# Optimization experiments

Hardware: AMD Instinct MI355X
Metric: run time of the kernel (lower is better)

Reference implementation:

```python
import jax, jax.numpy as jnp
import numpy as np

B, T, D, H = 2, 2048, 1024, 16
NEG = -65504.0


def setup_inputs() -> dict:
    key = jax.random.key(0)
    ks = jax.random.split(key, 12)
    std = float(np.sqrt(2.0 / (D + D)))  # xavier_normal for square weights
    inp = {
        'q': jax.random.normal(ks[0], (B, T, D), jnp.float32),
        'k': jax.random.normal(ks[1], (B, T, D), jnp.float32),
        'v': jax.random.normal(ks[2], (B, T, D), jnp.float32),
        'mask': jax.random.randint(ks[3], (B, T), 0, 2, jnp.int32),
        # weights stored as (in, out) so y = x @ W + b
        'Wq': jax.random.normal(ks[4], (D, D), jnp.float32) * std,
        'bq': jnp.zeros((D,), jnp.float32),
        'Wk': jax.random.normal(ks[5], (D, D), jnp.float32) * std,
        'bk': jnp.zeros((D,), jnp.float32),
        'Wv': jax.random.normal(ks[6], (D, D), jnp.float32) * std,
        'bv': jnp.zeros((D,), jnp.float32),
        'Wo': jax.random.normal(ks[7], (D, D), jnp.float32) * std,
        'bo': jnp.zeros((D,), jnp.float32),
    }
    return inp


def reference(q, k, v, mask, Wq, bq, Wk, bk, Wv, bv, Wo, bo):
    b, t, _ = q.shape
    dim_a = Wq.shape[1]
    dh = dim_a // H
    # projections, then split into heads: (b, t, H, dh)
    qh = (q @ Wq + bq).reshape(b, t, H, dh)
    kh = (k @ Wk + bk).reshape(b, t, H, dh)
    vh = (v @ Wv + bv).reshape(b, t, H, dh)
    # NOTE: module scales by 1/sqrt(dim_a) with the FULL dim_a, not per-head
    a = jnp.einsum('bthd,bshd->bhts', qh, kh) / jnp.sqrt(jnp.float32(dim_a))
    # 2D mask broadcasts over query positions: (b, 1, 1, t_keys)
    a = jnp.where(mask[:, None, None, :] == 0, NEG, a)
    a = jax.nn.softmax(a, axis=-1)  # dropout_prob=0 (eval mode)
    o = jnp.einsum('bhts,bshd->bthd', a, vh).reshape(b, t, dim_a)
    return o @ Wo + bo
```

## Files before the change

kernel.cpp:

```cpp
#include <hip/hip_runtime.h>
#include <hip/hip_bf16.h>
#include <math.h>

#define B_ 2
#define T_ 2048
#define D_ 1024
#define H_ 16
#define QSCALE (0.03125f * 1.44269504088896f)

typedef _Float16 f16;
using f16x4 = __attribute__((ext_vector_type(4))) _Float16;
using f16x8 = __attribute__((ext_vector_type(8))) _Float16;
using f32x4 = __attribute__((ext_vector_type(4))) float;

__device__ __forceinline__ void gl16(const void* g, void* l) {
  __builtin_amdgcn_global_load_lds(
      (__attribute__((address_space(1))) void*)g,
      (__attribute__((address_space(3))) void*)l, 16, 0, 0);
}

__global__ __launch_bounds__(256) void prep(
    const float* __restrict__ q, const float* __restrict__ k,
    const float* __restrict__ v, const int* __restrict__ mask,
    const float* __restrict__ Wq, const float* __restrict__ Wk,
    const float* __restrict__ Wv, const float* __restrict__ Wo,
    const float* __restrict__ bq, const float* __restrict__ bk,
    const float* __restrict__ bv, const float* __restrict__ bo,
    f16* __restrict__ xqkv, f16* __restrict__ Wt, float* __restrict__ bias,
    int* __restrict__ idx, int* __restrict__ inv, int* __restrict__ nk,
    f16* __restrict__ khc) {
  __shared__ float sh[64][65];
  const int bid = blockIdx.x;
  const int tid = threadIdx.x;

  if (bid < 6144) {
    const int z = bid / 2048;
    const float* src = (z == 0) ? q : (z == 1) ? k : v;
    const size_t i = ((size_t)(bid % 2048) * 256 + tid) * 8;
    float4 a = *(const float4*)(src + i);
    float4 b = *(const float4*)(src + i + 4);
    f16x8 o;
    o[0] = (f16)a.x; o[1] = (f16)a.y; o[2] = (f16)a.z; o[3] = (f16)a.w;
    o[4] = (f16)b.x; o[5] = (f16)b.y; o[6] = (f16)b.z; o[7] = (f16)b.w;
    *(f16x8*)(xqkv + (size_t)z * 4194304 + i) = o;
  } else if (bid < 7168) {
    const int id = bid - 6144;
    const int z = id >> 8;
    const int k0 = ((id >> 4) & 15) * 64, n0 = (id & 15) * 64;
    const float* W = (z == 0) ? Wq : (z == 1) ? Wk : (z == 2) ? Wv : Wo;
    const int r = tid >> 2, c0 = (tid & 3) * 16;
#pragma unroll
    for (int i = 0; i < 4; ++i)
      *(float4*)&sh[r][c0 + 4 * i] =
          *(const float4*)&W[(size_t)(k0 + r) * 1024 + n0 + c0 + 4 * i];
    __syncthreads();
    f16 tmp[16];
#pragma unroll
    for (int i = 0; i < 16; ++i) tmp[i] = (f16)sh[c0 + i][r];
    f16* dst = Wt + (size_t)z * 1048576 + (size_t)(n0 + r) * 1024 + k0 + c0;
    *(f16x8*)dst = *(f16x8*)&tmp[0];
    *(f16x8*)(dst + 8) = *(f16x8*)&tmp[8];
  } else if (bid < 7184) {
    const int i = (bid - 7168) * 256 + tid;
    const int z = i >> 10;
    const float* s = (z == 0) ? bq : (z == 1) ? bk : (z == 2) ? bv : bo;
    bias[i] = s[i & 1023];
  } else {
    const int b = bid - 7184;
    int* cnt = (int*)sh;
    int loc[8];
    int c = 0;
#pragma unroll
    for (int i = 0; i < 8; ++i) {
      loc[i] = mask[b * T_ + tid * 8 + i];
      c += loc[i];
    }
    cnt[tid] = c;
    __syncthreads();
    for (int off = 1; off < 256; off <<= 1) {
      int vsh = (tid >= off) ? cnt[tid - off] : 0;
      __syncthreads();
      cnt[tid] += vsh;
      __syncthreads();
    }
    int pos = cnt[tid] - c;
#pragma unroll
    for (int i = 0; i < 8; ++i) {
      const int t = tid * 8 + i;
      if (loc[i]) {
        idx[b * T_ + pos] = t;
        inv[b * T_ + t] = pos;
        ++pos;
      } else {
        inv[b * T_ + t] = -1;
      }
    }
    const int n = cnt[255];
    if (tid == 255) nk[b] = n;
    const int nkt = (n + 63) >> 6;
    const int npadrows = (nkt << 6) - n;
    uint4 z4 = {0u, 0u, 0u, 0u};
    f16* base = khc + ((size_t)b * T_ + n) * D_;
    for (int i = tid; i < npadrows * 128; i += 256)
      *(uint4*)(base + (size_t)i * 8) = z4;
  }
}

template <int TM, typename OT>
__global__ __launch_bounds__(256) void gemm_bt(
    const f16* __restrict__ Xb, const f16* __restrict__ Wtb,
    const float* __restrict__ biasb, void* __restrict__ C0,
    void* __restrict__ C1, void* __restrict__ C2,
    const int* __restrict__ inv, int M, int N, int K, float qscale) {
  constexpr int FM = TM / 32;
  __shared__ __align__(16) f16 As[TM * 32];
  __shared__ __align__(16) f16 Bs[128 * 32];
  const int z = blockIdx.z;
  const f16* X  = Xb  + (size_t)z * M * K;
  const f16* Wt = Wtb + (size_t)z * N * K;
  const float* bias = biasb + (size_t)z * N;
  OT* C = (OT*)((z == 0) ? C0 : (z == 1) ? C1 : C2);
  const float scl = (z == 0) ? qscale : 1.f;

  const int tid = threadIdx.x;
  const int wave = tid >> 6, lane = tid & 63;
  const int quad = lane >> 4, l16 = lane & 15;
  const int wm = wave & 1, wn = wave >> 1;
  const int m0 = blockIdx.y * TM, n0 = blockIdx.x * 128;

  f32x4 acc[FM][4] = {};

  const f16* asrc = X  + (size_t)(m0 + (tid >> 2)) * K + (tid & 3) * 8;
  const f16* bsrc = Wt + (size_t)(n0 + (tid >> 2)) * K + (tid & 3) * 8;
  char* aldst = (char*)As + tid * 16;
  char* bldst = (char*)Bs + tid * 16;
  const size_t rstep = (size_t)64 * K;

  const int NK = K >> 5;
  for (int kt = 0; kt < NK; ++kt) {
    if (kt) __syncthreads();
    gl16(asrc, aldst);
    if constexpr (TM == 128) gl16(asrc + rstep, aldst + 4096);
    gl16(bsrc, bldst);
    gl16(bsrc + rstep, bldst + 4096);
    asrc += 32; bsrc += 32;
    __syncthreads();

    f16x8 af[FM], bf[4];
#pragma unroll
    for (int t = 0; t < FM; ++t)
      af[t] = *(const f16x8*)&As[((TM / 2) * wm + 16 * t + l16) * 32 + quad * 8];
#pragma unroll
    for (int t = 0; t < 4; ++t)
      bf[t] = *(const f16x8*)&Bs[(64 * wn + 16 * t + l16) * 32 + quad * 8];
#pragma unroll
    for (int i = 0; i < FM; ++i)
#pragma unroll
      for (int j = 0; j < 4; ++j)
        acc[i][j] = __builtin_amdgcn_mfma_f32_16x16x32_f16(af[i], bf[j], acc[i][j], 0, 0, 0);
  }

  const int cm = m0 + (TM / 2) * wm + 4 * quad;
  const int cn = n0 + 64 * wn + l16;
  float bv[4];
#pragma unroll
  for (int tn = 0; tn < 4; ++tn) bv[tn] = bias[cn + 16 * tn];

  if (inv != nullptr && z == 1) {
    const int bb = m0 >> 11;
#pragma unroll
    for (int tm = 0; tm < FM; ++tm) {
#pragma unroll
      for (int r = 0; r < 4; ++r) {
        const int m = cm + 16 * tm + r;
        const int j = inv[m];
        if (j >= 0) {
          OT* row = C + ((size_t)(bb << 11) + j) * N;
#pragma unroll
          for (int tn = 0; tn < 4; ++tn)
            row[cn + 16 * tn] = (OT)(acc[tm][tn][r] + bv[tn]);
        }
      }
    }
  } else {
#pragma unroll
    for (int tm = 0; tm < FM; ++tm)
#pragma unroll
      for (int r = 0; r < 4; ++r) {
        OT* row = C + (size_t)(cm + 16 * tm + r) * N;
#pragma unroll
        for (int tn = 0; tn < 4; ++tn)
          row[cn + 16 * tn] = (OT)((acc[tm][tn][r] + bv[tn]) * scl);
      }
  }
}

__global__ __launch_bounds__(256) void vtrans(
    const f16* __restrict__ vh, const int* __restrict__ idx,
    const int* __restrict__ nk, f16* __restrict__ vhT) {
  const int tt = blockIdx.x, bh = blockIdx.y;
  const int b = bh >> 4, h = bh & 15;
  const int n = nk[b];
  const int nkt = (n + 63) >> 6;
  if (tt >= nkt) return;
  __shared__ f16 t[64][72];
  const int tid = threadIdx.x;
  const int r = tid >> 2, cq = 16 * (tid & 3);

  const int j = tt * 64 + r;
  uint4 v0 = {0u, 0u, 0u, 0u}, v1 = {0u, 0u, 0u, 0u};
  if (j < n) {
    const int tsrc = idx[b * T_ + j];
    const uint4* src = (const uint4*)(vh + ((size_t)b * T_ + tsrc) * D_ + h * 64 + cq);
    v0 = src[0]; v1 = src[1];
  }
  *(uint4*)&t[r][cq]     = v0;
  *(uint4*)&t[r][cq + 8] = v1;
  __syncthreads();

  f16 tmp[16];
#pragma unroll
  for (int xx = 0; xx < 16; ++xx) {
    int x = (xx + r) & 15;
    tmp[x] = t[cq + x][r];
  }
  f16* dst = vhT + ((size_t)bh * 64 + r) * T_ + tt * 64 + cq;
  *(uint4*)&dst[0] = *(uint4*)&tmp[0];
  *(uint4*)&dst[8] = *(uint4*)&tmp[8];
}

__global__ __launch_bounds__(256) void attn_mfma(
    const f16* __restrict__ qh, const f16* __restrict__ khc,
    const f16* __restrict__ vhT, const int* __restrict__ nkd,
    f16* __restrict__ oat) {
  __shared__ f16 Ks[64][72];
  __shared__ f16 Vt[64][72];
  __shared__ f16 Ps[4][32][72];

  const int qt = blockIdx.x, bh = blockIdx.y;
  const int b = bh >> 4, h = bh & 15;
  const int tid = threadIdx.x;
  const int wave = tid >> 6, lane = tid & 63;
  const int quad = lane >> 4, l16 = lane & 15;
  const int sr = tid >> 2, sq = 16 * (tid & 3);

  const int n = nkd[b];
  const int nkt = (n + 63) >> 6;
  const int npad = (nkt << 6) - n;

  f16x8 qf[2][2];
#pragma unroll
  for (int gq = 0; gq < 2; ++gq) {
    const f16* qp = qh + ((size_t)(b * T_ + qt * 128 + wave * 32 + 16 * gq + l16)) * D_ + h * 64 + quad * 8;
    qf[gq][0] = *(const f16x8*)qp;
    qf[gq][1] = *(const f16x8*)(qp + 32);
  }

  float lsum[2] = {0.f, 0.f};
  f32x4 o[2][4] = {};

  const f16* kbase = khc + (size_t)b * T_ * D_ + h * 64;
  const f16* vbase = vhT + ((size_t)bh * 64 + sr) * T_;

  uint4 kr0, kr1, vr0, vr1;
  auto load_kv = [&](int kt) {
    const uint4* ks = (const uint4*)(kbase + (size_t)(kt * 64 + sr) * D_ + sq);
    kr0 = ks[0]; kr1 = ks[1];
    const uint4* vs = (const uint4*)(vbase + kt * 64 + sq);
    vr0 = vs[0]; vr1 = vs[1];
  };
  if (nkt > 0) load_kv(0);

  for (int kt = 0; kt < nkt; ++kt) {
    *(uint4*)&Ks[sr][sq]     = kr0;
    *(uint4*)&Ks[sr][sq + 8] = kr1;
    *(uint4*)&Vt[sr][sq]     = vr0;
    *(uint4*)&Vt[sr][sq + 8] = vr1;
    __syncthreads();
    if (kt + 1 < nkt) load_kv(kt + 1);

#pragma unroll
    for (int tn = 0; tn < 4; ++tn) {
      f16x8 kf0 = *(const f16x8*)&Ks[16 * tn + l16][quad * 8];
      f16x8 kf1 = *(const f16x8*)&Ks[16 * tn + l16][32 + quad * 8];
#pragma unroll
      for (int gq = 0; gq < 2; ++gq) {
        f32x4 s = {0.f, 0.f, 0.f, 0.f};
        s = __builtin_amdgcn_mfma_f32_16x16x32_f16(kf0, qf[gq][0], s, 0, 0, 0);
        s = __builtin_amdgcn_mfma_f32_16x16x32_f16(kf1, qf[gq][1], s, 0, 0, 0);
        float p0 = exp2f(s[0]), p1 = exp2f(s[1]);
        float p2 = exp2f(s[2]), p3 = exp2f(s[3]);
        lsum[gq] += (p0 + p1) + (p2 + p3);
        f16x4 pk;
        pk[0] = (f16)p0; pk[1] = (f16)p1; pk[2] = (f16)p2; pk[3] = (f16)p3;
        *(f16x4*)&Ps[wave][16 * gq + l16][16 * tn + 4 * quad] = pk;
      }
    }

    f16x8 pf[2][2];
#pragma unroll
    for (int gq = 0; gq < 2; ++gq) {
      pf[gq][0] = *(const f16x8*)&Ps[wave][16 * gq + l16][quad * 8];
      pf[gq][1] = *(const f16x8*)&Ps[wave][16 * gq + l16][32 + quad * 8];
    }
#pragma unroll
    for (int t = 0; t < 4; ++t) {
      f16x8 vf0 = *(const f16x8*)&Vt[16 * t + l16][quad * 8];
      f16x8 vf1 = *(const f16x8*)&Vt[16 * t + l16][32 + quad * 8];
#pragma unroll
      for (int gq = 0; gq < 2; ++gq) {
        o[gq][t] = __builtin_amdgcn_mfma_f32_16x16x32_f16(pf[gq][0], vf0, o[gq][t], 0, 0, 0);
        o[gq][t] = __builtin_amdgcn_mfma_f32_16x16x32_f16(pf[gq][1], vf1, o[gq][t], 0, 0, 0);
      }
    }
    __syncthreads();
  }

#pragma unroll
  for (int gq = 0; gq < 2; ++gq) {
    float ls = lsum[gq];
    ls += __shfl_xor(ls, 16);
    ls += __shfl_xor(ls, 32);
    ls -= (float)npad;
    const size_t orow = (size_t)(b * T_ + qt * 128 + wave * 32 + 16 * gq + 4 * quad);
#pragma unroll
    for (int r = 0; r < 4; ++r) {
      const float iv = 1.f / __shfl(ls, 4 * quad + r);
#pragma unroll
      for (int t = 0; t < 4; ++t)
        oat[(orow + r) * D_ + h * 64 + 16 * t + l16] = (f16)(o[gq][t][r] * iv);
    }
  }
}

extern "C" void kernel_launch(void* const* d_in, const int* in_sizes, int n_in,
                              void* d_out, int out_size, void* d_ws, size_t ws_size,
                              hipStream_t stream) {
  const float* q  = (const float*)d_in[0];
  const float* k  = (const float*)d_in[1];
  const float* v  = (const float*)d_in[2];
  const int* mask = (const int*)d_in[3];
  const float* Wq = (const float*)d_in[4];
  const float* bq = (const float*)d_in[5];
  const float* Wk = (const float*)d_in[6];
  const float* bk = (const float*)d_in[7];
  const float* Wv = (const float*)d_in[8];
  const float* bv = (const float*)d_in[9];
  const float* Wo = (const float*)d_in[10];
  const float* bo = (const float*)d_in[11];
  float* out = (float*)d_out;

  char* ws = (char*)d_ws;
  f16* xqkv  = (f16*)(ws);
  f16* Wt    = (f16*)(ws + 25165824);
  f16* qh    = (f16*)(ws + 33554432);
  f16* vh    = (f16*)(ws + 41943040);
  f16* khc   = (f16*)(ws + 50331648);
  float* bsw = (float*)(ws + 58720256);
  int* idx   = (int*)(ws + 58736640);
  int* inv   = (int*)(ws + 58753024);
  int* nk    = (int*)(ws + 58769408);
  f16* vhT   = (f16*)(ws);
  f16* oat   = (f16*)(ws + 8388608);

  const int M = B_ * T_;
  dim3 blk(256);

  prep<<<dim3(7186), blk, 0, stream>>>(q, k, v, mask, Wq, Wk, Wv, Wo,
                                       bq, bk, bv, bo, xqkv, Wt, bsw,
                                       idx, inv, nk, khc);

  gemm_bt<128, f16><<<dim3(8, 32, 3), blk, 0, stream>>>(
      xqkv, Wt, bsw, qh, khc, vh, inv, M, D_, D_, QSCALE);

  vtrans<<<dim3(32, 32), blk, 0, stream>>>(vh, idx, nk, vhT);

  attn_mfma<<<dim3(16, 32), blk, 0, stream>>>(qh, khc, vhT, nk, oat);

  gemm_bt<64, float><<<dim3(8, 64, 1), blk, 0, stream>>>(
      oat, Wt + 3145728, bsw + 3072, out, out, out, nullptr, M, D_, D_, 1.f);
}
```

Baseline: 228.0 us.

## Fuse fp32-to-fp16 input cast into QKV GEMM and split attention keys in two

The QKV projection GEMM now reads fp32 activations directly, converting them to fp16 in registers while prefetching the next tile. This removes the separate cast pass over q/k/v and its workspace round trip. Attention is split into two key-range halves via a grid z dimension, doubling the block count. Each half writes unnormalized outputs and row sums, and the output GEMM merges the two partials and normalizes while loading its A tile. Because there is no running max, the partials can be added directly. The cost is extra partial-output traffic and A-tile loads that now go through registers instead of direct-to-LDS loads.

```diff
diff --git a/kernel.cpp b/kernel.cpp
--- a/kernel.cpp
+++ b/kernel.cpp
@@ -20,33 +20,21 @@
 }
 
 __global__ __launch_bounds__(256) void prep(
-    const float* __restrict__ q, const float* __restrict__ k,
-    const float* __restrict__ v, const int* __restrict__ mask,
+    const int* __restrict__ mask,
     const float* __restrict__ Wq, const float* __restrict__ Wk,
     const float* __restrict__ Wv, const float* __restrict__ Wo,
     const float* __restrict__ bq, const float* __restrict__ bk,
     const float* __restrict__ bv, const float* __restrict__ bo,
-    f16* __restrict__ xqkv, f16* __restrict__ Wt, float* __restrict__ bias,
+    f16* __restrict__ Wt, float* __restrict__ bias,
     int* __restrict__ idx, int* __restrict__ inv, int* __restrict__ nk,
     f16* __restrict__ khc) {
   __shared__ float sh[64][65];
   const int bid = blockIdx.x;
   const int tid = threadIdx.x;
 
-  if (bid < 6144) {
-    const int z = bid / 2048;
-    const float* src = (z == 0) ? q : (z == 1) ? k : v;
-    const size_t i = ((size_t)(bid % 2048) * 256 + tid) * 8;
-    float4 a = *(const float4*)(src + i);
-    float4 b = *(const float4*)(src + i + 4);
-    f16x8 o;
-    o[0] = (f16)a.x; o[1] = (f16)a.y; o[2] = (f16)a.z; o[3] = (f16)a.w;
-    o[4] = (f16)b.x; o[5] = (f16)b.y; o[6] = (f16)b.z; o[7] = (f16)b.w;
-    *(f16x8*)(xqkv + (size_t)z * 4194304 + i) = o;
-  } else if (bid < 7168) {
-    const int id = bid - 6144;
-    const int z = id >> 8;
-    const int k0 = ((id >> 4) & 15) * 64, n0 = (id & 15) * 64;
+  if (bid < 1024) {
+    const int z = bid >> 8;
+    const int k0 = ((bid >> 4) & 15) * 64, n0 = (bid & 15) * 64;
     const float* W = (z == 0) ? Wq : (z == 1) ? Wk : (z == 2) ? Wv : Wo;
     const int r = tid >> 2, c0 = (tid & 3) * 16;
 #pragma unroll
@@ -60,13 +48,13 @@
     f16* dst = Wt + (size_t)z * 1048576 + (size_t)(n0 + r) * 1024 + k0 + c0;
     *(f16x8*)dst = *(f16x8*)&tmp[0];
     *(f16x8*)(dst + 8) = *(f16x8*)&tmp[8];
-  } else if (bid < 7184) {
-    const int i = (bid - 7168) * 256 + tid;
+  } else if (bid < 1040) {
+    const int i = (bid - 1024) * 256 + tid;
     const int z = i >> 10;
     const float* s = (z == 0) ? bq : (z == 1) ? bk : (z == 2) ? bv : bo;
     bias[i] = s[i & 1023];
   } else {
-    const int b = bid - 7184;
+    const int b = bid - 1040;
     int* cnt = (int*)sh;
     int loc[8];
     int c = 0;
@@ -106,91 +94,106 @@
   }
 }
 
-template <int TM, typename OT>
-__global__ __launch_bounds__(256) void gemm_bt(
-    const f16* __restrict__ Xb, const f16* __restrict__ Wtb,
-    const float* __restrict__ biasb, void* __restrict__ C0,
-    void* __restrict__ C1, void* __restrict__ C2,
-    const int* __restrict__ inv, int M, int N, int K, float qscale) {
-  constexpr int FM = TM / 32;
-  __shared__ __align__(16) f16 As[TM * 32];
+__global__ __launch_bounds__(256) void gemm_qkv(
+    const float* __restrict__ xq, const float* __restrict__ xk,
+    const float* __restrict__ xv, const f16* __restrict__ Wtb,
+    const float* __restrict__ biasb, f16* __restrict__ qh,
+    f16* __restrict__ khc, f16* __restrict__ vh,
+    const int* __restrict__ inv) {
+  __shared__ __align__(16) f16 As[128 * 32];
   __shared__ __align__(16) f16 Bs[128 * 32];
   const int z = blockIdx.z;
-  const f16* X  = Xb  + (size_t)z * M * K;
-  const f16* Wt = Wtb + (size_t)z * N * K;
-  const float* bias = biasb + (size_t)z * N;
-  OT* C = (OT*)((z == 0) ? C0 : (z == 1) ? C1 : C2);
-  const float scl = (z == 0) ? qscale : 1.f;
+  const float* X = (z == 0) ? xq : (z == 1) ? xk : xv;
+  const f16* Wt = Wtb + (size_t)z * 1048576;
+  const float* bias = biasb + (size_t)z * 1024;
+  f16* C = (z == 0) ? qh : (z == 1) ? khc : vh;
 
   const int tid = threadIdx.x;
   const int wave = tid >> 6, lane = tid & 63;
   const int quad = lane >> 4, l16 = lane & 15;
   const int wm = wave & 1, wn = wave >> 1;
-  const int m0 = blockIdx.y * TM, n0 = blockIdx.x * 128;
-
-  f32x4 acc[FM][4] = {};
-
-  const f16* asrc = X  + (size_t)(m0 + (tid >> 2)) * K + (tid & 3) * 8;
-  const f16* bsrc = Wt + (size_t)(n0 + (tid >> 2)) * K + (tid & 3) * 8;
-  char* aldst = (char*)As + tid * 16;
+  const int m0 = blockIdx.y * 128, n0 = blockIdx.x * 128;
+
+  f32x4 acc[4][4] = {};
+
+  const float* asrc = X + (size_t)(m0 + (tid >> 2)) * 1024 + (tid & 3) * 8;
+  const f16* bsrc = Wt + (size_t)(n0 + (tid >> 2)) * 1024 + (tid & 3) * 8;
   char* bldst = (char*)Bs + tid * 16;
-  const size_t rstep = (size_t)64 * K;
-
-  const int NK = K >> 5;
-  for (int kt = 0; kt < NK; ++kt) {
+  f16* aw0 = As + tid * 8;
+  f16* aw1 = As + 2048 + tid * 8;
+
+  float ar[16];
+  auto loadA = [&](int k0) {
+    float4 x0 = *(const float4*)(asrc + k0);
+    float4 x1 = *(const float4*)(asrc + k0 + 4);
+    float4 x2 = *(const float4*)(asrc + 65536 + k0);
+    float4 x3 = *(const float4*)(asrc + 65536 + k0 + 4);
+    ar[0] = x0.x; ar[1] = x0.y; ar[2] = x0.z; ar[3] = x0.w;
+    ar[4] = x1.x; ar[5] = x1.y; ar[6] = x1.z; ar[7] = x1.w;
+    ar[8] = x2.x; ar[9] = x2.y; ar[10] = x2.z; ar[11] = x2.w;
+    ar[12] = x3.x; ar[13] = x3.y; ar[14] = x3.z; ar[15] = x3.w;
+  };
+  loadA(0);
+
+  for (int kt = 0; kt < 32; ++kt) {
     if (kt) __syncthreads();
-    gl16(asrc, aldst);
-    if constexpr (TM == 128) gl16(asrc + rstep, aldst + 4096);
     gl16(bsrc, bldst);
-    gl16(bsrc + rstep, bldst + 4096);
-    asrc += 32; bsrc += 32;
-    __syncthreads();
-
-    f16x8 af[FM], bf[4];
-#pragma unroll
-    for (int t = 0; t < FM; ++t)
-      af[t] = *(const f16x8*)&As[((TM / 2) * wm + 16 * t + l16) * 32 + quad * 8];
+    gl16(bsrc + 65536, bldst + 4096);
+    bsrc += 32;
+    f16x8 h0, h1;
+#pragma unroll
+    for (int i = 0; i < 8; ++i) { h0[i] = (f16)ar[i]; h1[i] = (f16)ar[8 + i]; }
+    *(f16x8*)aw0 = h0;
+    *(f16x8*)aw1 = h1;
+    __syncthreads();
+    if (kt + 1 < 32) loadA(32 * (kt + 1));
+
+    f16x8 af[4], bf[4];
+#pragma unroll
+    for (int t = 0; t < 4; ++t)
+      af[t] = *(const f16x8*)&As[(64 * wm + 16 * t + l16) * 32 + quad * 8];
 #pragma unroll
     for (int t = 0; t < 4; ++t)
       bf[t] = *(const f16x8*)&Bs[(64 * wn + 16 * t + l16) * 32 + quad * 8];
 #pragma unroll
-    for (int i = 0; i < FM; ++i)
+    for (int i = 0; i < 4; ++i)
 #pragma unroll
       for (int j = 0; j < 4; ++j)
         acc[i][j] = __builtin_amdgcn_mfma_f32_16x16x32_f16(af[i], bf[j], acc[i][j], 0, 0, 0);
   }
 
-  const int cm = m0 + (TM / 2) * wm + 4 * quad;
+  const int cm = m0 + 64 * wm + 4 * quad;
   const int cn = n0 + 64 * wn + l16;
   float bv[4];
 #pragma unroll
   for (int tn = 0; tn < 4; ++tn) bv[tn] = bias[cn + 16 * tn];
 
-  if (inv != nullptr && z == 1) {
+  if (z == 1) {
     const int bb = m0 >> 11;
 #pragma unroll
-    for (int tm = 0; tm < FM; ++tm) {
+    for (int tm = 0; tm < 4; ++tm) {
 #pragma unroll
       for (int r = 0; r < 4; ++r) {
         const int m = cm + 16 * tm + r;
         const int j = inv[m];
         if (j >= 0) {
-          OT* row = C + ((size_t)(bb << 11) + j) * N;
+          f16* row = C + ((size_t)(bb << 11) + j) * 1024;
 #pragma unroll
           for (int tn = 0; tn < 4; ++tn)
-            row[cn + 16 * tn] = (OT)(acc[tm][tn][r] + bv[tn]);
+            row[cn + 16 * tn] = (f16)(acc[tm][tn][r] + bv[tn]);
         }
       }
     }
   } else {
-#pragma unroll
-    for (int tm = 0; tm < FM; ++tm)
+    const float scl = (z == 0) ? QSCALE : 1.f;
+#pragma unroll
+    for (int tm = 0; tm < 4; ++tm)
 #pragma unroll
       for (int r = 0; r < 4; ++r) {
-        OT* row = C + (size_t)(cm + 16 * tm + r) * N;
+        f16* row = C + (size_t)(cm + 16 * tm + r) * 1024;
 #pragma unroll
         for (int tn = 0; tn < 4; ++tn)
-          row[cn + 16 * tn] = (OT)((acc[tm][tn][r] + bv[tn]) * scl);
+          row[cn + 16 * tn] = (f16)((acc[tm][tn][r] + bv[tn]) * scl);
       }
   }
 }
@@ -232,12 +235,12 @@
 __global__ __launch_bounds__(256) void attn_mfma(
     const f16* __restrict__ qh, const f16* __restrict__ khc,
     const f16* __restrict__ vhT, const int* __restrict__ nkd,
-    f16* __restrict__ oat) {
+    f16* __restrict__ opart, float* __restrict__ lpart) {
   __shared__ f16 Ks[64][72];
   __shared__ f16 Vt[64][72];
   __shared__ f16 Ps[4][32][72];
 
-  const int qt = blockIdx.x, bh = blockIdx.y;
+  const int qt = blockIdx.x, bh = blockIdx.y, ks = blockIdx.z;
   const int b = bh >> 4, h = bh & 15;
   const int tid = threadIdx.x;
   const int wave = tid >> 6, lane = tid & 63;
@@ -246,6 +249,10 @@
 
   const int n = nkd[b];
   const int nkt = (n + 63) >> 6;
+  const int hn = (nkt + 1) >> 1;
+  const int t_begin = ks ? hn : 0;
+  const int t_end = ks ? nkt : hn;
+  const bool owns_last = (t_end == nkt) && (t_end > t_begin);
   const int npad = (nkt << 6) - n;
 
   f16x8 qf[2][2];
@@ -264,20 +271,20 @@
 
   uint4 kr0, kr1, vr0, vr1;
   auto load_kv = [&](int kt) {
-    const uint4* ks = (const uint4*)(kbase + (size_t)(kt * 64 + sr) * D_ + sq);
-    kr0 = ks[0]; kr1 = ks[1];
-    const uint4* vs = (const uint4*)(vbase + kt * 64 + sq);
-    vr0 = vs[0]; vr1 = vs[1];
+    const uint4* kp = (const uint4*)(kbase + (size_t)(kt * 64 + sr) * D_ + sq);
+    kr0 = kp[0]; kr1 = kp[1];
+    const uint4* vp = (const uint4*)(vbase + kt * 64 + sq);
+    vr0 = vp[0]; vr1 = vp[1];
   };
-  if (nkt > 0) load_kv(0);
-
-  for (int kt = 0; kt < nkt; ++kt) {
+  if (t_begin < t_end) load_kv(t_begin);
+
+  for (int kt = t_begin; kt < t_end; ++kt) {
     *(uint4*)&Ks[sr][sq]     = kr0;
     *(uint4*)&Ks[sr][sq + 8] = kr1;
     *(uint4*)&Vt[sr][sq]     = vr0;
     *(uint4*)&Vt[sr][sq + 8] = vr1;
     __syncthreads();
-    if (kt + 1 < nkt) load_kv(kt + 1);
+    if (kt + 1 < t_end) load_kv(kt + 1);
 
 #pragma unroll
     for (int tn = 0; tn < 4; ++tn) {
@@ -316,20 +323,89 @@
     __syncthreads();
   }
 
+  f16* obase = opart + (size_t)ks * 4194304;
+  float* lbase = lpart + (size_t)ks * 65536 + (size_t)bh * 2048;
 #pragma unroll
   for (int gq = 0; gq < 2; ++gq) {
     float ls = lsum[gq];
     ls += __shfl_xor(ls, 16);
     ls += __shfl_xor(ls, 32);
-    ls -= (float)npad;
-    const size_t orow = (size_t)(b * T_ + qt * 128 + wave * 32 + 16 * gq + 4 * quad);
-#pragma unroll
-    for (int r = 0; r < 4; ++r) {
-      const float iv = 1.f / __shfl(ls, 4 * quad + r);
+    if (owns_last) ls -= (float)npad;
+    const int qrow0 = qt * 128 + wave * 32 + 16 * gq;
+    if (quad == 0) lbase[qrow0 + l16] = ls;
+    const size_t orow = (size_t)(b * T_ + qrow0 + 4 * quad);
+#pragma unroll
+    for (int r = 0; r < 4; ++r)
 #pragma unroll
       for (int t = 0; t < 4; ++t)
-        oat[(orow + r) * D_ + h * 64 + 16 * t + l16] = (f16)(o[gq][t][r] * iv);
-    }
+        obase[(orow + r) * D_ + h * 64 + 16 * t + l16] = (f16)o[gq][t][r];
+  }
+}
+
+__global__ __launch_bounds__(256) void gemm_out(
+    const f16* __restrict__ opart, const float* __restrict__ lpart,
+    const f16* __restrict__ Wt3, const float* __restrict__ bias3,
+    float* __restrict__ out) {
+  __shared__ __align__(16) f16 As[64 * 32];
+  __shared__ __align__(16) f16 Bs[128 * 32];
+  const int tid = threadIdx.x;
+  const int wave = tid >> 6, lane = tid & 63;
+  const int quad = lane >> 4, l16 = lane & 15;
+  const int wm = wave & 1, wn = wave >> 1;
+  const int m0 = blockIdx.y * 64, n0 = blockIdx.x * 128;
+
+  f32x4 acc[2][4] = {};
+
+  const int row = m0 + (tid >> 2);
+  const int cq = (tid & 3) * 8;
+  const f16* oa = opart + (size_t)row * 1024 + cq;
+  const f16* ob = oa + 4194304;
+  const float* lp = lpart + (size_t)(row >> 11) * 32768 + (row & 2047);
+  const f16* bsrc = Wt3 + (size_t)(n0 + (tid >> 2)) * 1024 + cq;
+  char* bldst = (char*)Bs + tid * 16;
+
+  for (int kt = 0; kt < 32; ++kt) {
+    if (kt) __syncthreads();
+    gl16(bsrc, bldst);
+    gl16(bsrc + 65536, bldst + 4096);
+    bsrc += 32;
+    const int h = (kt * 32 + cq) >> 6;
+    const float la = lp[h * 2048];
+    const float lb = lp[65536 + h * 2048];
+    const float invl = 1.f / (la + lb);
+    f16x8 a8 = *(const f16x8*)(oa + kt * 32);
+    f16x8 b8 = *(const f16x8*)(ob + kt * 32);
+    f16x8 hv;
+#pragma unroll
+    for (int i = 0; i < 8; ++i)
+      hv[i] = (f16)(((float)a8[i] + (float)b8[i]) * invl);
+    *(f16x8*)(As + tid * 8) = hv;
+    __syncthreads();
+
+    f16x8 af[2], bf[4];
+#pragma unroll
+    for (int t = 0; t < 2; ++t)
+      af[t] = *(const f16x8*)&As[(32 * wm + 16 * t + l16) * 32 + quad * 8];
+#pragma unroll
+    for (int t = 0; t < 4; ++t)
+      bf[t] = *(const f16x8*)&Bs[(64 * wn + 16 * t + l16) * 32 + quad * 8];
+#pragma unroll
+    for (int i = 0; i < 2; ++i)
+#pragma unroll
+      for (int j = 0; j < 4; ++j)
+        acc[i][j] = __builtin_amdgcn_mfma_f32_16x16x32_f16(af[i], bf[j], acc[i][j], 0, 0, 0);
+  }
+
+  const int cm = m0 + 32 * wm + 4 * quad;
+  const int cn = n0 + 64 * wn + l16;
+#pragma unroll
+  for (int tn = 0; tn < 4; ++tn) {
+    const float bv = bias3[cn + 16 * tn];
+#pragma unroll
+    for (int tm = 0; tm < 2; ++tm)
+#pragma unroll
+      for (int r = 0; r < 4; ++r)
+        out[(size_t)(cm + 16 * tm + r) * 1024 + cn + 16 * tn] = acc[tm][tn][r] + bv;
   }
 }
 
@@ -351,32 +427,31 @@
   float* out = (float*)d_out;
 
   char* ws = (char*)d_ws;
-  f16* xqkv  = (f16*)(ws);
-  f16* Wt    = (f16*)(ws + 25165824);
-  f16* qh    = (f16*)(ws + 33554432);
-  f16* vh    = (f16*)(ws + 41943040);
-  f16* khc   = (f16*)(ws + 50331648);
-  float* bsw = (float*)(ws + 58720256);
-  int* idx   = (int*)(ws + 58736640);
-  int* inv   = (int*)(ws + 58753024);
-  int* nk    = (int*)(ws + 58769408);
-  f16* vhT   = (f16*)(ws);
-  f16* oat   = (f16*)(ws + 8388608);
-
-  const int M = B_ * T_;
+  f16* qh     = (f16*)(ws);
+  f16* vh     = (f16*)(ws + 8388608);
+  f16* khc    = (f16*)(ws + 16777216);
+  f16* vhT    = (f16*)(ws + 25165824);
+  f16* opart  = (f16*)(ws + 33554432);
+  f16* Wt     = (f16*)(ws + 50331648);
+  float* lpart = (float*)(ws + 58720256);
+  float* bsw  = (float*)(ws + 59244544);
+  int* idx    = (int*)(ws + 59260928);
+  int* inv    = (int*)(ws + 59277312);
+  int* nk     = (int*)(ws + 59293696);
+
   dim3 blk(256);
 
-  prep<<<dim3(7186), blk, 0, stream>>>(q, k, v, mask, Wq, Wk, Wv, Wo,
-                                       bq, bk, bv, bo, xqkv, Wt, bsw,
-                                       idx, inv, nk, khc);
-
-  gemm_bt<128, f16><<<dim3(8, 32, 3), blk, 0, stream>>>(
-      xqkv, Wt, bsw, qh, khc, vh, inv, M, D_, D_, QSCALE);
+  prep<<<dim3(1042), blk, 0, stream>>>(mask, Wq, Wk, Wv, Wo, bq, bk, bv, bo,
+                                       Wt, bsw, idx, inv, nk, khc);
+
+  gemm_qkv<<<dim3(8, 32, 3), blk, 0, stream>>>(q, k, v, Wt, bsw,
+                                               qh, khc, vh, inv);
 
   vtrans<<<dim3(32, 32), blk, 0, stream>>>(vh, idx, nk, vhT);
 
-  attn_mfma<<<dim3(16, 32), blk, 0, stream>>>(qh, khc, vhT, nk, oat);
-
-  gemm_bt<64, float><<<dim3(8, 64, 1), blk, 0, stream>>>(
-      oat, Wt + 3145728, bsw + 3072, out, out, out, nullptr, M, D_, D_, 1.f);
-}
+  attn_mfma<<<dim3(16, 32, 2), blk, 0, stream>>>(qh, khc, vhT, nk,
+                                                 opart, lpart);
+
+  gemm_out<<<dim3(8, 64), blk, 0, stream>>>(opart, lpart, Wt + 3145728,
+                                            bsw + 3072, out);
+}
```

New measurement: 246.7 us. 1.08x slower.
